# Kernel optimization log

Measured on AMD Instinct MI355X. Metric: run time of the kernel, lower is better.

## Reference

```python
import jax, jax.numpy as jnp
import numpy as np

N = 4096          # number_of_node
DIN = 3           # dim_input (forced: fc1 expects N*dim_input == N*3 after last stage)
DOUT = 4          # dim_output
DACT = N          # dim_action defaults to number_of_node
B = 128


def setup_inputs() -> dict:
    key = jax.random.key(0)
    ks = jax.random.split(key, 12)
    X = jax.random.normal(ks[0], (B, N * DIN), dtype=jnp.float32)
    adj = jax.random.uniform(ks[1], (N, N), dtype=jnp.float32)
    def lin(kw, kb, fan_in, fan_out):
        bound = 1.0 / np.sqrt(fan_in)
        W = jax.random.uniform(kw, (fan_in, fan_out), minval=-bound, maxval=bound, dtype=jnp.float32)
        b = jax.random.uniform(kb, (fan_out,), minval=-bound, maxval=bound, dtype=jnp.float32)
        return W, b
    W1, b1 = lin(ks[2], ks[3], DIN, 4)
    W2, b2 = lin(ks[4], ks[5], 4, DOUT)
    W3, b3 = lin(ks[6], ks[7], DOUT, 3)
    Wfc, bfc = lin(ks[8], ks[9], N * DIN, 54)
    Wout, bout = lin(ks[10], ks[11], 54, DACT)
    return {"X": X, "adj": adj, "W1": W1, "b1": b1, "W2": W2, "b2": b2,
            "W3": W3, "b3": b3, "Wfc": Wfc, "bfc": bfc, "Wout": Wout, "bout": bout}


def reference(X, adj, W1, b1, W2, b2, W3, b3, Wfc, bfc, Wout, bout):
    # X: [B, N*DIN] -> [B, N, DIN]
    h = X.reshape(X.shape[0], N, DIN)
    # three (adj @ h) aggregations fused with tiny Linear + ReLU
    h = jax.nn.relu(jnp.einsum('nm,bmf->bnf', adj, h) @ W1 + b1)   # [B,N,4]
    h = jax.nn.relu(jnp.einsum('nm,bmf->bnf', adj, h) @ W2 + b2)   # [B,N,DOUT]
    h = jax.nn.relu(jnp.einsum('nm,bmf->bnf', adj, h) @ W3 + b3)   # [B,N,3]
    flat = h.reshape(h.shape[0], -1)                               # [B, N*3]
    hid = jax.nn.relu(flat @ Wfc + bfc)                            # [B, 54]
    q_value = hid @ Wout + bout                                    # [B, DACT]
    return q_value
```

## Files before the change

kernel.cpp:

```cpp
#include <hip/hip_runtime.h>


typedef __bf16 bf16x8 __attribute__((ext_vector_type(8)));
typedef float  f32x4  __attribute__((ext_vector_type(4)));

#define N_NODE 4096
#define BATCH  128

__device__ __forceinline__ void async_copy16(const void* gsrc, void* ldst) {
    __builtin_amdgcn_global_load_lds(
        (const __attribute__((address_space(1))) void*)gsrc,
        (__attribute__((address_space(3))) void*)ldst,
        16, 0, 0);
}

__global__ __launch_bounds__(256) void prep_k(const float* __restrict__ adj,
                                              __bf16* __restrict__ adjB,
                                              const float* __restrict__ X,
                                              const float* __restrict__ W1,
                                              __bf16* __restrict__ G0,
                                              float* __restrict__ hid_acc) {
    const int blk = blockIdx.x, tx = threadIdx.x;
    if (blk < 8192) {
        const size_t i = (size_t)blk * 256 + tx;
        const float4* a4 = (const float4*)adj;
        float4 u = a4[i * 2];
        float4 v = a4[i * 2 + 1];
        bf16x8 o = { (__bf16)u.x, (__bf16)u.y, (__bf16)u.z, (__bf16)u.w,
                     (__bf16)v.x, (__bf16)v.y, (__bf16)v.z, (__bf16)v.w };
        *(bf16x8*)(adjB + i * 8) = o;
    } else if (blk < 10240) {
        const int base = (blk - 8192) * 1024;
        const int c = base >> 12, b = c >> 2, f = c & 3;
        const float w0 = W1[0 * 4 + f], w1 = W1[1 * 4 + f], w2 = W1[2 * 4 + f];
        const float* Xb = X + (size_t)b * 12288;
#pragma unroll
        for (int k = 0; k < 4; ++k) {
            const int idx = base + k * 256 + tx;
            const int m = idx & 4095;
            const float v = Xb[m * 3 + 0] * w0 + Xb[m * 3 + 1] * w1 + Xb[m * 3 + 2] * w2;
            G0[idx] = (__bf16)v;
        }
    } else {
        const int i = (blk - 10240) * 256 + tx;
        if (i < BATCH * 54) hid_acc[i] = 0.f;
    }
}

template <int MODE>
__global__ __launch_bounds__(256) void gcn_k(const __bf16* __restrict__ A,
                                             const __bf16* __restrict__ Bt,
                                             const float* __restrict__ Wa,
                                             const float* __restrict__ ba,
                                             const float* __restrict__ Wb,
                                             __bf16* __restrict__ Hout,
                                             float* __restrict__ H3out) {
    __shared__ __align__(16) __bf16 smem[2][2][2][2048];
    const int tx   = threadIdx.x;
    const int wave = tx >> 6, lane = tx & 63;
    const int quad = lane >> 4, lr = lane & 15;

    const int l = blockIdx.x;
    const int xcd = l & 7, s = l >> 3;
    const int mi = xcd * 8 + (s & 7), ci = s >> 3;
    const int m0 = mi * 64, c0 = ci * 64;
    const int wm = wave >> 1, wn = wave & 1;

    const int srow   = tx >> 2;
    const int schunk = ((tx & 3) - (srow >> 1)) & 3;
    const int skoff  = schunk * 8;
    const __bf16* gA = A  + (size_t)(m0 + srow) * 4096 + skoff;
    const __bf16* gB = Bt + (size_t)(c0 + srow) * 4096 + skoff;
    __bf16* lA0_ = &smem[0][0][0][tx * 8];  __bf16* lA1_ = &smem[0][0][1][tx * 8];
    __bf16* lB0_ = &smem[1][0][0][tx * 8];  __bf16* lB1_ = &smem[1][0][1][tx * 8];
    const int bufstride = 4096;

    const int pos = (quad + (lr >> 1)) & 3;
    const int arow0 = (wm * 32 + lr) * 32 + pos * 8;
    const int brow0 = (wn * 32 + lr) * 32 + pos * 8;

    f32x4 acc[2][2] = {};

    async_copy16(gA,      lA0_);
    async_copy16(gA + 32, lA1_);
    async_copy16(gB,      lB0_);
    async_copy16(gB + 32, lB1_);

    int buf = 0;
    for (int kt = 0; kt < 64; ++kt) {
        __syncthreads();
        if (kt + 1 < 64) {
            const int ko = (kt + 1) * 64;
            const int bo = (buf ^ 1) * bufstride;
            async_copy16(gA + ko,      lA0_ + bo);
            async_copy16(gA + ko + 32, lA1_ + bo);
            async_copy16(gB + ko,      lB0_ + bo);
            async_copy16(gB + ko + 32, lB1_ + bo);
        }
#pragma unroll
        for (int kh = 0; kh < 2; ++kh) {
            bf16x8 a0  = *(const bf16x8*)(&smem[0][buf][kh][arow0]);
            bf16x8 a1  = *(const bf16x8*)(&smem[0][buf][kh][arow0 + 512]);
            bf16x8 b0v = *(const bf16x8*)(&smem[1][buf][kh][brow0]);
            bf16x8 b1v = *(const bf16x8*)(&smem[1][buf][kh][brow0 + 512]);
            acc[0][0] = __builtin_amdgcn_mfma_f32_16x16x32_bf16(a0, b0v, acc[0][0], 0, 0, 0);
            acc[0][1] = __builtin_amdgcn_mfma_f32_16x16x32_bf16(a0, b1v, acc[0][1], 0, 0, 0);
            acc[1][0] = __builtin_amdgcn_mfma_f32_16x16x32_bf16(a1, b0v, acc[1][0], 0, 0, 0);
            acc[1][1] = __builtin_amdgcn_mfma_f32_16x16x32_bf16(a1, b1v, acc[1][1], 0, 0, 0);
        }
        buf ^= 1;
    }

    __syncthreads();
    float* Ct = (float*)smem;
#pragma unroll
    for (int i = 0; i < 2; ++i)
#pragma unroll
        for (int j = 0; j < 2; ++j)
#pragma unroll
            for (int r = 0; r < 4; ++r)
                Ct[(wm * 32 + i * 16 + quad * 4 + r) * 65 + wn * 32 + j * 16 + lr] = acc[i][j][r];
    __syncthreads();

    const int m_l = tx & 63, bq = tx >> 6;
    if (MODE == 0) {
        const float b0f = ba[0], b1f = ba[1], b2f = ba[2], b3f = ba[3];
#pragma unroll
        for (int q = 0; q < 4; ++q) {
            const int bl = bq * 4 + q;
            const float* row = &Ct[m_l * 65 + bl * 4];
            __bf16* o = Hout + (size_t)(c0 + bl * 4) * N_NODE + m0 + m_l;
            o[0 * N_NODE] = (__bf16)fmaxf(row[0] + b0f, 0.f);
            o[1 * N_NODE] = (__bf16)fmaxf(row[1] + b1f, 0.f);
            o[2 * N_NODE] = (__bf16)fmaxf(row[2] + b2f, 0.f);
            o[3 * N_NODE] = (__bf16)fmaxf(row[3] + b3f, 0.f);
        }
    } else if (MODE == 1) {
        float W2l[16], W3l[12], bl2[4];
#pragma unroll
        for (int i = 0; i < 16; ++i) W2l[i] = Wa[i];
#pragma unroll
        for (int i = 0; i < 12; ++i) W3l[i] = Wb[i];
#pragma unroll
        for (int i = 0; i < 4; ++i) bl2[i] = ba[i];
#pragma unroll
        for (int q = 0; q < 4; ++q) {
            const int bl = bq * 4 + q;
            const float* row = &Ct[m_l * 65 + bl * 4];
            float tmp[4];
#pragma unroll
            for (int fo = 0; fo < 4; ++fo)
                tmp[fo] = fmaxf(row[0] * W2l[fo] + row[1] * W2l[4 + fo] +
                                row[2] * W2l[8 + fo] + row[3] * W2l[12 + fo] + bl2[fo], 0.f);
            __bf16* o = Hout + (size_t)(c0 + bl * 4) * N_NODE + m0 + m_l;
#pragma unroll
            for (int f3 = 0; f3 < 3; ++f3)
                o[f3 * N_NODE] = (__bf16)(tmp[0] * W3l[f3] + tmp[1] * W3l[3 + f3] +
                                          tmp[2] * W3l[6 + f3] + tmp[3] * W3l[9 + f3]);
            o[3 * N_NODE] = (__bf16)0.f;
        }
    } else {
        const float b0f = ba[0], b1f = ba[1], b2f = ba[2];
#pragma unroll
        for (int q = 0; q < 4; ++q) {
            const int bl = bq * 4 + q;
            const int b = ci * 16 + bl;
            const float* row = &Ct[m_l * 65 + bl * 4];
            float* o = H3out + (size_t)(b * 3) * N_NODE + m0 + m_l;
            o[0 * N_NODE] = fmaxf(row[0] + b0f, 0.f);
            o[1 * N_NODE] = fmaxf(row[1] + b1f, 0.f);
            o[2 * N_NODE] = fmaxf(row[2] + b2f, 0.f);
        }
    }
}

__global__ __launch_bounds__(256) void fc1p_k(const float* __restrict__ H3,
                                              const float* __restrict__ Wfc,
                                              float* __restrict__ hid_acc) {
    __shared__ float hs[16 * 192];
    __shared__ float red[4][16][64];
    const int tx = threadIdx.x;
    const int wv = tx >> 6, lane = tx & 63;
    const int n0 = blockIdx.x * 64;
    const int b0 = blockIdx.y * 16;

    for (int idx = tx; idx < 3072; idx += 256) {
        const int n = idx & 63, f = (idx >> 6) % 3, b = idx / 192;
        hs[idx] = H3[((size_t)((b0 + b) * 3 + f)) * N_NODE + n0 + n];
    }
    __syncthreads();

    float acc[16];
#pragma unroll
    for (int b = 0; b < 16; ++b) acc[b] = 0.f;
    if (lane < 54) {
        const int nb = wv * 16;
        for (int n = 0; n < 16; ++n) {
#pragma unroll
            for (int f = 0; f < 3; ++f) {
                const float w = Wfc[((size_t)(n0 + nb + n) * 3 + f) * 54 + lane];
#pragma unroll
                for (int b = 0; b < 16; ++b)
                    acc[b] += hs[b * 192 + f * 64 + nb + n] * w;
            }
        }
    }
#pragma unroll
    for (int b = 0; b < 16; ++b) red[wv][b][lane] = acc[b];
    __syncthreads();
    if (wv == 0 && lane < 54) {
        for (int b = 0; b < 16; ++b) {
            const float s = red[0][b][lane] + red[1][b][lane] +
                            red[2][b][lane] + red[3][b][lane];
            atomicAdd(&hid_acc[(b0 + b) * 54 + lane], s);
        }
    }
}

__global__ __launch_bounds__(256) void fc2_k(const float* __restrict__ hid_acc,
                                             const float* __restrict__ bfc,
                                             const float* __restrict__ Wout,
                                             const float* __restrict__ bout,
                                             float* __restrict__ out) {
    const int tx = threadIdx.x;
    const int a  = blockIdx.x * 256 + tx;
    const int b0 = blockIdx.y * 4;
    __shared__ float hs[4 * 54];
    if (tx < 216) {
        const int j = tx % 54;
        hs[tx] = fmaxf(hid_acc[b0 * 54 + tx] + bfc[j], 0.f);
    }
    __syncthreads();
    float a0 = 0.f, a1 = 0.f, a2 = 0.f, a3 = 0.f;
    for (int j = 0; j < 54; ++j) {
        float w = Wout[(size_t)j * N_NODE + a];
        a0 += hs[0 * 54 + j] * w;
        a1 += hs[1 * 54 + j] * w;
        a2 += hs[2 * 54 + j] * w;
        a3 += hs[3 * 54 + j] * w;
    }
    float bo = bout[a];
    out[(size_t)(b0 + 0) * N_NODE + a] = a0 + bo;
    out[(size_t)(b0 + 1) * N_NODE + a] = a1 + bo;
    out[(size_t)(b0 + 2) * N_NODE + a] = a2 + bo;
    out[(size_t)(b0 + 3) * N_NODE + a] = a3 + bo;
}

extern "C" void kernel_launch(void* const* d_in, const int* in_sizes, int n_in,
                              void* d_out, int out_size, void* d_ws, size_t ws_size,
                              hipStream_t stream) {
    const float* X    = (const float*)d_in[0];
    const float* adj  = (const float*)d_in[1];
    const float* W1   = (const float*)d_in[2];
    const float* b1   = (const float*)d_in[3];
    const float* W2   = (const float*)d_in[4];
    const float* b2   = (const float*)d_in[5];
    const float* W3   = (const float*)d_in[6];
    const float* b3   = (const float*)d_in[7];
    const float* Wfc  = (const float*)d_in[8];
    const float* bfc  = (const float*)d_in[9];
    const float* Wout = (const float*)d_in[10];
    const float* bout = (const float*)d_in[11];
    float* out = (float*)d_out;

    char* w = (char*)d_ws;
    __bf16* adjB = (__bf16*)w;
    __bf16* G0   = (__bf16*)(w + 33554432);
    __bf16* H1   = (__bf16*)(w + 33554432 + 4194304);
    __bf16* H2g  = (__bf16*)(w + 33554432 + 2 * 4194304);
    float*  H3   = (float*)(w + 33554432 + 3 * 4194304);
    float*  hid  = (float*)(w + 33554432 + 3 * 4194304 + 6291456);

    prep_k<<<10267, 256, 0, stream>>>(adj, adjB, X, W1, G0, hid);

    gcn_k<0><<<512, 256, 0, stream>>>(adjB, G0, nullptr, b1, nullptr, H1, nullptr);
    gcn_k<1><<<512, 256, 0, stream>>>(adjB, H1, W2, b2, W3, H2g, nullptr);
    gcn_k<2><<<512, 256, 0, stream>>>(adjB, H2g, nullptr, b3, nullptr, nullptr, H3);

    fc1p_k<<<dim3(64, 8), 256, 0, stream>>>(H3, Wfc, hid);
    fc2_k<<<dim3(16, 32), 256, 0, stream>>>(hid, bfc, Wout, bout, out);
}
```

Measured before the change: 233.7 us.

## Split K across waves with 128-wide K tiles and reduce partials in LDS

The GCN matmul kernel now loads 128-wide K slices per stage instead of 64, using a 16-chunk swizzle and a 64KB LDS buffer. Each wave computes the full 64x64 output tile over its own quarter of each K slice (split-K within the block), and the four waves' partial accumulators are summed through LDS before the epilogue. This halves the loop iterations and barriers and lets each wave reuse its A and B fragments across a 4x4 grid of MFMAs, which should raise MFMA density. In exchange, each wave holds 64 accumulator registers, LDS use grows to 64KB (which may cut occupancy), and the epilogue adds a cross-wave reduction step.

New measurement: 226.5 us. 3.0% less time.

```diff
diff --git a/kernel.cpp b/kernel.cpp
--- a/kernel.cpp
+++ b/kernel.cpp
@@ -55,7 +55,7 @@
                                              const float* __restrict__ Wb,
                                              __bf16* __restrict__ Hout,
                                              float* __restrict__ H3out) {
-    __shared__ __align__(16) __bf16 smem[2][2][2][2048];
+    __shared__ __align__(16) unsigned char smem[65536];
     const int tx   = threadIdx.x;
     const int wave = tx >> 6, lane = tx & 63;
     const int quad = lane >> 4, lr = lane & 15;
@@ -64,62 +64,85 @@
     const int xcd = l & 7, s = l >> 3;
     const int mi = xcd * 8 + (s & 7), ci = s >> 3;
     const int m0 = mi * 64, c0 = ci * 64;
-    const int wm = wave >> 1, wn = wave & 1;
-
-    const int srow   = tx >> 2;
-    const int schunk = ((tx & 3) - (srow >> 1)) & 3;
-    const int skoff  = schunk * 8;
-    const __bf16* gA = A  + (size_t)(m0 + srow) * 4096 + skoff;
-    const __bf16* gB = Bt + (size_t)(c0 + srow) * 4096 + skoff;
-    __bf16* lA0_ = &smem[0][0][0][tx * 8];  __bf16* lA1_ = &smem[0][0][1][tx * 8];
-    __bf16* lB0_ = &smem[1][0][0][tx * 8];  __bf16* lB1_ = &smem[1][0][1][tx * 8];
-    const int bufstride = 4096;
-
-    const int pos = (quad + (lr >> 1)) & 3;
-    const int arow0 = (wm * 32 + lr) * 32 + pos * 8;
-    const int brow0 = (wn * 32 + lr) * 32 + pos * 8;
-
-    f32x4 acc[2][2] = {};
-
-    async_copy16(gA,      lA0_);
-    async_copy16(gA + 32, lA1_);
-    async_copy16(gB,      lB0_);
-    async_copy16(gB + 32, lB1_);
+
+    const __bf16* gA[4];
+    const __bf16* gB[4];
+#pragma unroll
+    for (int q = 0; q < 4; ++q) {
+        const int c = q * 256 + tx;
+        const int r = c >> 4, p = c & 15;
+        const int lk = (p - (r & 15)) & 15;
+        gA[q] = A  + (size_t)(m0 + r) * 4096 + lk * 8;
+        gB[q] = Bt + (size_t)(c0 + r) * 4096 + lk * 8;
+    }
+
+    const int posw = ((wave * 4 + quad + lr) & 15) * 8;
+    int foff[4];
+#pragma unroll
+    for (int g = 0; g < 4; ++g) foff[g] = (g * 16 + lr) * 128 + posw;
+
+    f32x4 acc[4][4] = {};
+
+#pragma unroll
+    for (int q = 0; q < 4; ++q) {
+        async_copy16(gA[q], smem + q * 4096 + tx * 16);
+        async_copy16(gB[q], smem + 16384 + q * 4096 + tx * 16);
+    }
 
     int buf = 0;
-    for (int kt = 0; kt < 64; ++kt) {
+    for (int kt = 0; kt < 32; ++kt) {
         __syncthreads();
-        if (kt + 1 < 64) {
-            const int ko = (kt + 1) * 64;
-            const int bo = (buf ^ 1) * bufstride;
-            async_copy16(gA + ko,      lA0_ + bo);
-            async_copy16(gA + ko + 32, lA1_ + bo);
-            async_copy16(gB + ko,      lB0_ + bo);
-            async_copy16(gB + ko + 32, lB1_ + bo);
-        }
-#pragma unroll
-        for (int kh = 0; kh < 2; ++kh) {
-            bf16x8 a0  = *(const bf16x8*)(&smem[0][buf][kh][arow0]);
-            bf16x8 a1  = *(const bf16x8*)(&smem[0][buf][kh][arow0 + 512]);
-            bf16x8 b0v = *(const bf16x8*)(&smem[1][buf][kh][brow0]);
-            bf16x8 b1v = *(const bf16x8*)(&smem[1][buf][kh][brow0 + 512]);
-            acc[0][0] = __builtin_amdgcn_mfma_f32_16x16x32_bf16(a0, b0v, acc[0][0], 0, 0, 0);
-            acc[0][1] = __builtin_amdgcn_mfma_f32_16x16x32_bf16(a0, b1v, acc[0][1], 0, 0, 0);
-            acc[1][0] = __builtin_amdgcn_mfma_f32_16x16x32_bf16(a1, b0v, acc[1][0], 0, 0, 0);
-            acc[1][1] = __builtin_amdgcn_mfma_f32_16x16x32_bf16(a1, b1v, acc[1][1], 0, 0, 0);
-        }
+        if (kt + 1 < 32) {
+            const int k0 = (kt + 1) * 128;
+            const int bo = (buf ^ 1) * 32768;
+#pragma unroll
+            for (int q = 0; q < 4; ++q) {
+                async_copy16(gA[q] + k0, smem + bo + q * 4096 + tx * 16);
+                async_copy16(gB[q] + k0, smem + bo + 16384 + q * 4096 + tx * 16);
+            }
+        }
+        const __bf16* Ab = (const __bf16*)(smem + buf * 32768);
+        const __bf16* Bb = (const __bf16*)(smem + buf * 32768 + 16384);
+        bf16x8 af[4], bv[4];
+#pragma unroll
+        for (int i = 0; i < 4; ++i) af[i] = *(const bf16x8*)(Ab + foff[i]);
+#pragma unroll
+        for (int j = 0; j < 4; ++j) bv[j] = *(const bf16x8*)(Bb + foff[j]);
+#pragma unroll
+        for (int i = 0; i < 4; ++i)
+#pragma unroll
+            for (int j = 0; j < 4; ++j)
+                acc[i][j] = __builtin_amdgcn_mfma_f32_16x16x32_bf16(af[i], bv[j], acc[i][j], 0, 0, 0);
         buf ^= 1;
     }
 
     __syncthreads();
-    float* Ct = (float*)smem;
-#pragma unroll
-    for (int i = 0; i < 2; ++i)
-#pragma unroll
-        for (int j = 0; j < 2; ++j)
-#pragma unroll
-            for (int r = 0; r < 4; ++r)
-                Ct[(wm * 32 + i * 16 + quad * 4 + r) * 65 + wn * 32 + j * 16 + lr] = acc[i][j][r];
+    float* part = (float*)smem;
+    if (wave != 0) {
+        float* slot = part + (wave - 1) * 4096;
+#pragma unroll
+        for (int t = 0; t < 16; ++t)
+            *(f32x4*)(slot + lane * 64 + ((t + lane) & 15) * 4) = acc[t >> 2][t & 3];
+    }
+    __syncthreads();
+    float* Ct = (float*)(smem + 32768);
+    if (wave == 0) {
+#pragma unroll
+        for (int t = 0; t < 16; ++t) {
+            const int o = lane * 64 + ((t + lane) & 15) * 4;
+            f32x4 p0 = *(const f32x4*)(part + o);
+            f32x4 p1 = *(const f32x4*)(part + 4096 + o);
+            f32x4 p2 = *(const f32x4*)(part + 8192 + o);
+            acc[t >> 2][t & 3] += p0 + p1 + p2;
+        }
+#pragma unroll
+        for (int i = 0; i < 4; ++i)
+#pragma unroll
+            for (int j = 0; j < 4; ++j)
+#pragma unroll
+                for (int r = 0; r < 4; ++r)
+                    Ct[(i * 16 + quad * 4 + r) * 65 + j * 16 + lr] = acc[i][j][r];
+    }
     __syncthreads();
 
     const int m_l = tx & 63, bq = tx >> 6;
```
